# Kernel tuning notes

Hardware: AMD Instinct MI355X
Metric: run time of the kernel (lower is better)

## Reference

```python
import jax, jax.numpy as jnp
import numpy as np

B, T, D, U, ORDER = 128, 256, 256, 512, 512  # batch, time, input_dims, units, ladder state order


def setup_inputs() -> dict:
    key = jax.random.key(0)
    ks = jax.random.split(key, 9)
    inputs = jax.random.normal(ks[0], (B, T, D), jnp.float32)
    # trainable weights
    wfm = jax.random.normal(ks[1], (D,), jnp.float32) * 0.1
    WyhT = jax.random.normal(ks[2], (U, U), jnp.float32) / np.sqrt(U)
    WyxT = jax.random.normal(ks[3], (ORDER, U), jnp.float32) / np.sqrt(ORDER)
    WyfT = jax.random.normal(ks[4], (D, U), jnp.float32) / np.sqrt(D)
    by = jnp.zeros((U,), jnp.float32)
    # frozen ladder state-space matrices (Constant initializers in the original);
    # scaled for a stable linear recurrence over T steps
    AT = jax.random.normal(ks[5], (ORDER, ORDER), jnp.float32) * (0.9 / np.sqrt(ORDER))
    BT = jax.random.normal(ks[6], (D, ORDER), jnp.float32) / np.sqrt(D)
    CT = jax.random.normal(ks[7], (ORDER, D), jnp.float32) / np.sqrt(ORDER)
    return {"inputs": inputs, "wfm": wfm, "WyhT": WyhT, "WyxT": WyxT,
            "WyfT": WyfT, "by": by, "AT": AT, "BT": BT, "CT": CT}


def reference(inputs, wfm, WyhT, WyxT, WyfT, by, AT, BT, CT):
    b = inputs.shape[0]
    h0 = jnp.zeros((b, U), inputs.dtype)
    m0 = jnp.zeros((b, D), inputs.dtype)
    x0 = jnp.zeros((b, ORDER), inputs.dtype)

    def step(carry, inp_t):
        h, m, x = carry
        u = inp_t + m                      # [b, D]
        x = x @ AT + u @ BT                # [b, ORDER] linear state update
        m = x @ CT                         # [b, D]     memory readout
        f = wfm * m                        # [b, D]     gated memory feature
        h = jnp.tanh(h @ WyhT + x @ WyxT + f @ WyfT + by)  # [b, U]
        return (h, m, x), h

    _, hs = jax.lax.scan(step, (h0, m0, x0), jnp.swapaxes(inputs, 0, 1))
    return jnp.swapaxes(hs, 0, 1)          # [b, T, U]
```

## Files before the change

### kernel.cpp

```cpp
#include <hip/hip_runtime.h>
#include <math.h>

#define BB 128
#define TT 256
#define DD 256
#define UU 512
#define RR 512

#define OFF_X0 0
#define OFF_X1 65536
#define OFF_M  131072
#define OFF_HZ 163840
#define WS_FLT 229376
#define WS_NEED_BYTES (WS_FLT * 4)

__global__ __launch_bounds__(256) void zero_kernel(float* __restrict__ p, int n)
{
    int i = blockIdx.x * 256 + threadIdx.x;
    if (i < n) p[i] = 0.0f;
}

__global__ __launch_bounds__(256) void combo_kernel(
    const float* __restrict__ inputs, const float* __restrict__ wfm,
    const float* __restrict__ by,     const float* __restrict__ WyhT,
    const float* __restrict__ WyxT,   const float* __restrict__ WyfT,
    const float* __restrict__ AT,     const float* __restrict__ BT,
    const float* __restrict__ xin,
    const float* __restrict__ m,
    const float* __restrict__ hz,
    float* __restrict__ xout,
    float* __restrict__ out, int t)
{
    const int bid  = blockIdx.x;
    const int lane = threadIdx.x & 63;
    const int wv   = threadIdx.x >> 6;
    const int cg   = bid & 7;
    const int grp  = bid >> 3;
    const bool is_x = grp < 16;
    const int rg   = grp & 15;
    const int c    = cg * 64 + lane;
    const int r0   = rg * 8 + wv * 2;

    if (is_x) {
        if (t > TT - 2 && t != -1) return;
        if (t >= TT - 1) return;
        const float* x0 = xin + r0 * RR;
        const float* x1 = x0 + RR;
        float a0 = 0.0f, a1 = 0.0f;
        #pragma unroll 16
        for (int k = 0; k < RR; ++k) {
            float w = AT[k * RR + c];
            a0 = fmaf(x0[k], w, a0);
            a1 = fmaf(x1[k], w, a1);
        }
        const float* i0 = inputs + (r0 * TT + (t + 1)) * DD;
        const float* i1 = i0 + TT * DD;
        const float* m0 = m + r0 * DD;
        const float* m1 = m0 + DD;
        float b0 = 0.0f, b1 = 0.0f;
        #pragma unroll 16
        for (int d = 0; d < DD; ++d) {
            float w  = BT[d * RR + c];
            float u0 = i0[d] + m0[d];
            float u1 = i1[d] + m1[d];
            b0 = fmaf(u0, w, b0);
            b1 = fmaf(u1, w, b1);
        }
        xout[r0 * RR + c]       = a0 + b0;
        xout[(r0 + 1) * RR + c] = a1 + b1;
    } else {
        if (t < 0) return;
        const float* h0 = (t == 0) ? (hz + r0 * UU) : (out + (r0 * TT + (t - 1)) * UU);
        const float* h1 = (t == 0) ? (h0 + UU)      : (h0 + TT * UU);
        const float* x0 = xin + r0 * RR;
        const float* x1 = x0 + RR;
        float accH0 = 0.0f, accH1 = 0.0f, accX0 = 0.0f, accX1 = 0.0f;
        #pragma unroll 8
        for (int k = 0; k < UU; ++k) {
            float wh = WyhT[k * UU + c];
            float wx = WyxT[k * UU + c];
            accH0 = fmaf(h0[k], wh, accH0);
            accH1 = fmaf(h1[k], wh, accH1);
            accX0 = fmaf(x0[k], wx, accX0);
            accX1 = fmaf(x1[k], wx, accX1);
        }
        const float* m0 = m + r0 * DD;
        const float* m1 = m0 + DD;
        float accF0 = 0.0f, accF1 = 0.0f;
        #pragma unroll 16
        for (int d = 0; d < DD; ++d) {
            float w  = WyfT[d * UU + c];
            float f0 = wfm[d] * m0[d];
            float f1 = wfm[d] * m1[d];
            accF0 = fmaf(f0, w, accF0);
            accF1 = fmaf(f1, w, accF1);
        }
        float z0 = ((accH0 + accX0) + accF0) + by[c];
        float z1 = ((accH1 + accX1) + accF1) + by[c];
        out[(r0 * TT + t) * UU + c]       = tanhf(z0);
        out[((r0 + 1) * TT + t) * UU + c] = tanhf(z1);
    }
}

__global__ __launch_bounds__(256) void m_kernel(
    const float* __restrict__ CT, const float* __restrict__ x,
    float* __restrict__ m)
{
    const int bid  = blockIdx.x;
    const int lane = threadIdx.x & 63;
    const int wv   = threadIdx.x >> 6;
    const int cg   = bid & 7;
    const int rg   = bid >> 3;
    const int row  = rg * 8 + wv * 2 + (lane >> 5);
    const int c    = cg * 32 + (lane & 31);
    const float* xr = x + row * RR;
    float acc = 0.0f;
    #pragma unroll 16
    for (int k = 0; k < RR; ++k)
        acc = fmaf(xr[k], CT[k * DD + c], acc);
    m[row * DD + c] = acc;
}

__global__ __launch_bounds__(64) void sentinel_kernel(float* __restrict__ out, float v)
{
    if (threadIdx.x == 0 && blockIdx.x == 0) out[0] = v;
}

extern "C" void kernel_launch(void* const* d_in, const int* in_sizes, int n_in,
                              void* d_out, int out_size, void* d_ws, size_t ws_size,
                              hipStream_t stream)
{
    const float* inputs = (const float*)d_in[0];
    const float* wfm    = (const float*)d_in[1];
    const float* WyhT   = (const float*)d_in[2];
    const float* WyxT   = (const float*)d_in[3];
    const float* WyfT   = (const float*)d_in[4];
    const float* by     = (const float*)d_in[5];
    const float* AT     = (const float*)d_in[6];
    const float* BT     = (const float*)d_in[7];
    const float* CT     = (const float*)d_in[8];
    float* out = (float*)d_out;
    float* ws  = (float*)d_ws;

    double code = 0.0;
    static const int exp_sizes[9] = {8388608, 256, 262144, 262144, 131072,
                                     512, 262144, 131072, 131072};
    if (n_in != 9) {
        code = 3.0e6 + n_in;
    } else {
        for (int i = 0; i < 9; ++i)
            if (in_sizes[i] != exp_sizes[i]) { code = 2.0e6 + i * 1.0e4; break; }
    }
    if (code == 0.0 && out_size != BB * TT * UU)
        code = 4.0e6 + (double)(out_size / 10000);
    if (code == 0.0 && ws_size < (size_t)WS_NEED_BYTES)
        code = 1.0e6 + (double)(ws_size / 1024);
    if (code != 0.0) {
        sentinel_kernel<<<1, 64, 0, stream>>>(out, (float)code);
        return;
    }

    float* X0 = ws + OFF_X0;
    float* X1 = ws + OFF_X1;
    float* M  = ws + OFF_M;
    float* HZ = ws + OFF_HZ;

    zero_kernel<<<(WS_FLT + 255) / 256, 256, 0, stream>>>(ws, WS_FLT);

    combo_kernel<<<256, 256, 0, stream>>>(inputs, wfm, by, WyhT, WyxT, WyfT, AT, BT,
                                          X1, M, HZ, X0, out, -1);
    m_kernel<<<128, 256, 0, stream>>>(CT, X0, M);

    for (int t = 0; t < TT - 1; ++t) {
        float* xc = (t & 1) ? X1 : X0;
        float* xn = (t & 1) ? X0 : X1;
        combo_kernel<<<256, 256, 0, stream>>>(inputs, wfm, by, WyhT, WyxT, WyfT, AT, BT,
                                              xc, M, HZ, xn, out, t);
        m_kernel<<<128, 256, 0, stream>>>(CT, xn, M);
    }
    combo_kernel<<<256, 256, 0, stream>>>(inputs, wfm, by, WyhT, WyxT, WyfT, AT, BT,
                                          X1, M, HZ, X0, out, TT - 1);
}
```

Measured before the change: 12.66 ms.

## Fuse memory readout into step kernel using atomic counters and double-buffered M

Removes the separate m_kernel launch per timestep. Its x@CT readout now runs in 64 extra blocks of the combined step kernel, which spin-wait on per-row-group atomic counters until the x-update blocks for those rows have finished. M is double-buffered so the h-update blocks can read the current m while the next m is being written. This roughly halves the number of kernel launches and lets the m computation overlap with the h update. The cost is a spin-wait that relies on all 320 blocks being co-resident, and extra global-memory synchronization.

```diff
diff --git a/kernel.cpp b/kernel.cpp
--- a/kernel.cpp
+++ b/kernel.cpp
@@ -9,9 +9,11 @@
 
 #define OFF_X0 0
 #define OFF_X1 65536
-#define OFF_M  131072
-#define OFF_HZ 163840
-#define WS_FLT 229376
+#define OFF_M0 131072
+#define OFF_M1 163840
+#define OFF_HZ 196608
+#define OFF_CN 262144
+#define WS_FLT 262160
 #define WS_NEED_BYTES (WS_FLT * 4)
 
 __global__ __launch_bounds__(256) void zero_kernel(float* __restrict__ p, int n)
@@ -25,51 +27,26 @@
     const float* __restrict__ by,     const float* __restrict__ WyhT,
     const float* __restrict__ WyxT,   const float* __restrict__ WyfT,
     const float* __restrict__ AT,     const float* __restrict__ BT,
+    const float* __restrict__ CT,
     const float* __restrict__ xin,
-    const float* __restrict__ m,
+    const float* __restrict__ mc,
     const float* __restrict__ hz,
-    float* __restrict__ xout,
+    float* __restrict__ xn,
+    float* __restrict__ mn,
+    unsigned int* __restrict__ cnt,
     float* __restrict__ out, int t)
 {
     const int bid  = blockIdx.x;
-    const int lane = threadIdx.x & 63;
-    const int wv   = threadIdx.x >> 6;
-    const int cg   = bid & 7;
-    const int grp  = bid >> 3;
-    const bool is_x = grp < 16;
-    const int rg   = grp & 15;
-    const int c    = cg * 64 + lane;
-    const int r0   = rg * 8 + wv * 2;
+    const int tid  = threadIdx.x;
+    const int lane = tid & 63;
+    const int wv   = tid >> 6;
 
-    if (is_x) {
-        if (t > TT - 2 && t != -1) return;
-        if (t >= TT - 1) return;
-        const float* x0 = xin + r0 * RR;
-        const float* x1 = x0 + RR;
-        float a0 = 0.0f, a1 = 0.0f;
-        #pragma unroll 16
-        for (int k = 0; k < RR; ++k) {
-            float w = AT[k * RR + c];
-            a0 = fmaf(x0[k], w, a0);
-            a1 = fmaf(x1[k], w, a1);
-        }
-        const float* i0 = inputs + (r0 * TT + (t + 1)) * DD;
-        const float* i1 = i0 + TT * DD;
-        const float* m0 = m + r0 * DD;
-        const float* m1 = m0 + DD;
-        float b0 = 0.0f, b1 = 0.0f;
-        #pragma unroll 16
-        for (int d = 0; d < DD; ++d) {
-            float w  = BT[d * RR + c];
-            float u0 = i0[d] + m0[d];
-            float u1 = i1[d] + m1[d];
-            b0 = fmaf(u0, w, b0);
-            b1 = fmaf(u1, w, b1);
-        }
-        xout[r0 * RR + c]       = a0 + b0;
-        xout[(r0 + 1) * RR + c] = a1 + b1;
-    } else {
+    if (bid < 128) {
         if (t < 0) return;
+        const int cg_ = bid & 7;
+        const int rg  = bid >> 3;
+        const int c   = cg_ * 64 + lane;
+        const int r0  = rg * 8 + wv * 2;
         const float* h0 = (t == 0) ? (hz + r0 * UU) : (out + (r0 * TT + (t - 1)) * UU);
         const float* h1 = (t == 0) ? (h0 + UU)      : (h0 + TT * UU);
         const float* x0 = xin + r0 * RR;
@@ -84,7 +61,7 @@
             accX0 = fmaf(x0[k], wx, accX0);
             accX1 = fmaf(x1[k], wx, accX1);
         }
-        const float* m0 = m + r0 * DD;
+        const float* m0 = mc + r0 * DD;
         const float* m1 = m0 + DD;
         float accF0 = 0.0f, accF1 = 0.0f;
         #pragma unroll 16
@@ -99,26 +76,66 @@
         float z1 = ((accH1 + accX1) + accF1) + by[c];
         out[(r0 * TT + t) * UU + c]       = tanhf(z0);
         out[((r0 + 1) * TT + t) * UU + c] = tanhf(z1);
+    } else if (bid < 256) {
+        if (t >= TT - 1) return;
+        const int b   = bid - 128;
+        const int cg_ = b & 7;
+        const int rg  = b >> 3;
+        const int c   = cg_ * 64 + lane;
+        const int r0  = rg * 8 + wv * 2;
+        const float* x0 = xin + r0 * RR;
+        const float* x1 = x0 + RR;
+        float a0 = 0.0f, a1 = 0.0f;
+        #pragma unroll 16
+        for (int k = 0; k < RR; ++k) {
+            float w = AT[k * RR + c];
+            a0 = fmaf(x0[k], w, a0);
+            a1 = fmaf(x1[k], w, a1);
+        }
+        const float* i0 = inputs + (r0 * TT + (t + 1)) * DD;
+        const float* i1 = i0 + TT * DD;
+        const float* m0 = mc + r0 * DD;
+        const float* m1 = m0 + DD;
+        float b0 = 0.0f, b1 = 0.0f;
+        #pragma unroll 16
+        for (int d = 0; d < DD; ++d) {
+            float w  = BT[d * RR + c];
+            float u0 = i0[d] + m0[d];
+            float u1 = i1[d] + m1[d];
+            b0 = fmaf(u0, w, b0);
+            b1 = fmaf(u1, w, b1);
+        }
+        xn[r0 * RR + c]       = a0 + b0;
+        xn[(r0 + 1) * RR + c] = a1 + b1;
+        __syncthreads();
+        if (tid == 0)
+            __hip_atomic_fetch_add(&cnt[rg], 1u, __ATOMIC_RELEASE,
+                                   __HIP_MEMORY_SCOPE_AGENT);
+    } else {
+        if (t >= TT - 1) return;
+        const int g  = bid - 256;
+        const int r0 = g * 2;
+        const int rg = r0 >> 3;
+        const unsigned int tgt = 8u * (unsigned int)(t + 2);
+        if (tid == 0) {
+            while (__hip_atomic_load(&cnt[rg], __ATOMIC_ACQUIRE,
+                                     __HIP_MEMORY_SCOPE_AGENT) < tgt)
+                __builtin_amdgcn_s_sleep(1);
+        }
+        __syncthreads();
+        const int c = tid;
+        const float* xr0 = xn + r0 * RR;
+        const float* xr1 = xr0 + RR;
+        float a0 = 0.0f, a1 = 0.0f;
+        #pragma unroll 16
+        for (int k = 0; k < RR; ++k) {
+            float w = CT[k * DD + c];
+            a0 = fmaf(xr0[k], w, a0);
+            a1 = fmaf(xr1[k], w, a1);
+        }
+        mn[r0 * DD + c]       = a0;
+        mn[(r0 + 1) * DD + c] = a1;
     }
-}
-
-__global__ __launch_bounds__(256) void m_kernel(
-    const float* __restrict__ CT, const float* __restrict__ x,
-    float* __restrict__ m)
-{
-    const int bid  = blockIdx.x;
-    const int lane = threadIdx.x & 63;
-    const int wv   = threadIdx.x >> 6;
-    const int cg   = bid & 7;
-    const int rg   = bid >> 3;
-    const int row  = rg * 8 + wv * 2 + (lane >> 5);
-    const int c    = cg * 32 + (lane & 31);
-    const float* xr = x + row * RR;
-    float acc = 0.0f;
-    #pragma unroll 16
-    for (int k = 0; k < RR; ++k)
-        acc = fmaf(xr[k], CT[k * DD + c], acc);
-    m[row * DD + c] = acc;
 }
 
 __global__ __launch_bounds__(64) void sentinel_kernel(float* __restrict__ out, float v)
@@ -162,22 +179,20 @@
 
     float* X0 = ws + OFF_X0;
     float* X1 = ws + OFF_X1;
-    float* M  = ws + OFF_M;
+    float* M0 = ws + OFF_M0;
+    float* M1 = ws + OFF_M1;
     float* HZ = ws + OFF_HZ;
+    unsigned int* CN = reinterpret_cast<unsigned int*>(ws + OFF_CN);
 
     zero_kernel<<<(WS_FLT + 255) / 256, 256, 0, stream>>>(ws, WS_FLT);
 
-    combo_kernel<<<256, 256, 0, stream>>>(inputs, wfm, by, WyhT, WyxT, WyfT, AT, BT,
-                                          X1, M, HZ, X0, out, -1);
-    m_kernel<<<128, 256, 0, stream>>>(CT, X0, M);
-
-    for (int t = 0; t < TT - 1; ++t) {
-        float* xc = (t & 1) ? X1 : X0;
-        float* xn = (t & 1) ? X0 : X1;
-        combo_kernel<<<256, 256, 0, stream>>>(inputs, wfm, by, WyhT, WyxT, WyfT, AT, BT,
-                                              xc, M, HZ, xn, out, t);
-        m_kernel<<<128, 256, 0, stream>>>(CT, xn, M);
+    for (int t = -1; t < TT; ++t) {
+        const float* xc = (t & 1) ? X1 : X0;
+        float*       xnp = (t & 1) ? X0 : X1;
+        const float* mcp = (t & 1) ? M1 : M0;
+        float*       mnp = (t & 1) ? M0 : M1;
+        combo_kernel<<<320, 256, 0, stream>>>(inputs, wfm, by, WyhT, WyxT, WyfT,
+                                              AT, BT, CT, xc, mcp, HZ, xnp, mnp,
+                                              CN, out, t);
     }
-    combo_kernel<<<256, 256, 0, stream>>>(inputs, wfm, by, WyhT, WyxT, WyfT, AT, BT,
-                                          X1, M, HZ, X0, out, TT - 1);
 }
```

Result: slower. 26.11 ms (+106.3%).
